# Kernel tuning notes

Hardware: AMD Instinct MI355X
Metric: run time of the kernel (lower is better)

## Reference

```python
import jax, jax.numpy as jnp
import numpy as np

N_NODES = 100000
N_EDGES = 1600000
IN_C, HID_C, OUT_C = 128, 128, 64


def setup_inputs() -> dict:
    key = jax.random.key(0)
    k = jax.random.split(key, 5)
    x = jax.random.normal(k[0], (N_NODES, IN_C), dtype=jnp.float32)
    edge_index = jax.random.randint(k[1], (2, N_EDGES), 0, N_NODES, dtype=jnp.int32)
    # Glorot-ish scaling for the GCNConv linear weights
    W1 = jax.random.normal(k[2], (IN_C, HID_C), dtype=jnp.float32) * (1.0 / np.sqrt(IN_C))
    b1 = jnp.zeros((HID_C,), dtype=jnp.float32)
    W2 = jax.random.normal(k[3], (HID_C, OUT_C), dtype=jnp.float32) * (1.0 / np.sqrt(HID_C))
    b2 = jnp.zeros((OUT_C,), dtype=jnp.float32)
    return {"x": x, "edge_index": edge_index, "W1": W1, "b1": b1, "W2": W2, "b2": b2}


def _gcn_conv(h, W, b, src, dst, deg_inv_sqrt, n):
    # h: [N, F_in] -> linear transform, then deg-normalized scatter-add over edges
    h = h @ W  # [N, F_out]
    norm = deg_inv_sqrt[src] * deg_inv_sqrt[dst]  # [E+N] (self-loops included)
    msgs = h[src] * norm[:, None]  # gather + scale
    out = jax.ops.segment_sum(msgs, dst, num_segments=n)  # scatter-add to dst
    return out + b


def reference(x, edge_index, W1, b1, W2, b2):
    n = x.shape[0]
    loops = jnp.arange(n, dtype=edge_index.dtype)
    src = jnp.concatenate([edge_index[0], loops])  # add self-loops (PyG default)
    dst = jnp.concatenate([edge_index[1], loops])
    deg = jax.ops.segment_sum(jnp.ones_like(dst, dtype=x.dtype), dst, num_segments=n)
    deg_inv_sqrt = jax.lax.rsqrt(deg)  # deg >= 1 due to self-loops

    h = _gcn_conv(x, W1, b1, src, dst, deg_inv_sqrt, n)
    h = jax.nn.relu(h)
    # F.dropout(training=False) is identity at inference
    h = _gcn_conv(h, W2, b2, src, dst, deg_inv_sqrt, n)
    return jax.nn.log_softmax(h, axis=1)
```

## Files before the change

### kernel.cpp

```cpp
#include <hip/hip_runtime.h>
#include <hip/hip_bf16.h>


typedef unsigned short ushortT;
typedef unsigned char ucharT;
typedef __attribute__((ext_vector_type(8))) short short8v;
typedef __attribute__((ext_vector_type(4))) float float4v;
typedef __attribute__((ext_vector_type(2))) float float2v;
typedef __attribute__((ext_vector_type(8))) unsigned short ushort8v;

__device__ __forceinline__ float bf2f(ushortT u) {
  union { unsigned int i; float f; } x;
  x.i = ((unsigned int)u) << 16;
  return x.f;
}

__device__ __forceinline__ ushortT f2bf(float f) {
  __hip_bfloat16 h = __float2bfloat16(f);
  return *(ushortT*)&h;
}

__device__ __forceinline__ ucharT f2fp8(float f) {
  unsigned int w = __builtin_amdgcn_cvt_pk_fp8_f32(f, f, 0, false);
  return (ucharT)(w & 0xff);
}

__device__ __forceinline__ void fp8x8_to_f32(unsigned int lo, unsigned int hi,
                                             float* f) {
  float2v p0 = __builtin_amdgcn_cvt_pk_f32_fp8(lo, false);
  float2v p1 = __builtin_amdgcn_cvt_pk_f32_fp8(lo, true);
  float2v p2 = __builtin_amdgcn_cvt_pk_f32_fp8(hi, false);
  float2v p3 = __builtin_amdgcn_cvt_pk_f32_fp8(hi, true);
  f[0] = p0[0]; f[1] = p0[1]; f[2] = p1[0]; f[3] = p1[1];
  f[4] = p2[0]; f[5] = p2[1]; f[6] = p3[0]; f[7] = p3[1];
}

__device__ __forceinline__ void fp8x4_to_f32(unsigned int w, float* f) {
  float2v p0 = __builtin_amdgcn_cvt_pk_f32_fp8(w, false);
  float2v p1 = __builtin_amdgcn_cvt_pk_f32_fp8(w, true);
  f[0] = p0[0]; f[1] = p0[1]; f[2] = p1[0]; f[3] = p1[1];
}

__device__ __forceinline__ bool probe_isbf(const void* xv) {
  const ushortT* xr = (const ushortT*)xv;
  const int lane = threadIdx.x & 63;
  float v = bf2f(xr[lane]);
  bool sane = isfinite(v) && fabsf(v) < 1e4f;
  return __ballot(sane) == ~0ull;
}

__global__ __launch_bounds__(256) void wprep_k(const void* __restrict__ W1v,
                                               const void* __restrict__ W2v,
                                               const void* __restrict__ xv,
                                               ushortT* __restrict__ Wt1,
                                               ushortT* __restrict__ Wt2) {
  const bool isbf = probe_isbf(xv);
  const int i = blockIdx.x * 256 + threadIdx.x;
  if (i < 16384) {
    int nn = i & 127, k = i >> 7;
    ushortT v = isbf ? ((const ushortT*)W1v)[k * 128 + nn]
                     : f2bf(((const float*)W1v)[k * 128 + nn]);
    Wt1[nn * 128 + k] = v;
  } else if (i < 24576) {
    int j = i - 16384;
    int nn = j & 63, k = j >> 6;
    ushortT v = isbf ? ((const ushortT*)W2v)[k * 64 + nn]
                     : f2bf(((const float*)W2v)[k * 64 + nn]);
    Wt2[nn * 128 + k] = v;
  }
}


__global__ __launch_bounds__(256) void bhist_k(const int* __restrict__ dst, int E, int B,
                                               int* __restrict__ gbc) {
  __shared__ int h[512];
  const int tid = threadIdx.x;
  for (int i = tid; i < B; i += 256) h[i] = 0;
  __syncthreads();
  const int i0 = blockIdx.x * 8192;
  const int iend = min(i0 + 8192, E);
  for (int i = i0 + tid; i < iend; i += 256) atomicAdd(&h[dst[i] >> 8], 1);
  __syncthreads();
  for (int i = tid; i < B; i += 256)
    if (h[i]) atomicAdd(&gbc[i], h[i]);
}

__global__ __launch_bounds__(256) void bscan_k(const int* __restrict__ gbc, int B,
                                               int* __restrict__ bbase,
                                               int* __restrict__ gcur) {
  __shared__ int p[256];
  const int t = threadIdx.x;
  int a = (2 * t < B) ? gbc[2 * t] : 0;
  int b = (2 * t + 1 < B) ? gbc[2 * t + 1] : 0;
  const int sum = a + b;
  p[t] = sum;
  __syncthreads();
  int run = sum;
  for (int off = 1; off < 256; off <<= 1) {
    int v = (t >= off) ? p[t - off] : 0;
    __syncthreads();
    run += v;
    p[t] = run;
    __syncthreads();
  }
  const int excl = run - sum;
  if (2 * t < B) { bbase[2 * t] = excl; gcur[2 * t] = excl; }
  if (2 * t + 1 < B) { bbase[2 * t + 1] = excl + a; gcur[2 * t + 1] = excl + a; }
}

__global__ __launch_bounds__(256) void bin_k(const int* __restrict__ srcv,
                                             const int* __restrict__ dstv, int E, int B,
                                             int* __restrict__ gcur,
                                             int* __restrict__ tmp) {
  __shared__ int hist[512];
  __shared__ int base[512];
  const int tid = threadIdx.x;
  const int i0 = blockIdx.x * 8192;
  const int iend = min(i0 + 8192, E);
  for (int i = tid; i < B; i += 256) hist[i] = 0;
  __syncthreads();
  for (int i = i0 + tid; i < iend; i += 256) atomicAdd(&hist[dstv[i] >> 8], 1);
  __syncthreads();
  for (int i = tid; i < B; i += 256) {
    int h = hist[i];
    base[i] = h ? atomicAdd(&gcur[i], h) : 0;
    hist[i] = 0;
  }
  __syncthreads();
  for (int i = i0 + tid; i < iend; i += 256) {
    int d = dstv[i];
    int s = srcv[i];
    int b = d >> 8;
    int l = atomicAdd(&hist[b], 1);
    tmp[base[b] + l] = s | ((d & 255) << 17);
  }
}

__global__ __launch_bounds__(256) void csr_k(const int* __restrict__ tmp,
                                             const int* __restrict__ bbase,
                                             const int* __restrict__ gbc, int n,
                                             int2* __restrict__ rpc,
                                             float* __restrict__ dis,
                                             int* __restrict__ col) {
  __shared__ int lhist[256];
  __shared__ int lexcl[256];
  const int b = blockIdx.x;
  const int tid = threadIdx.x;
  const int e0 = bbase[b];
  const int e1 = e0 + gbc[b];
  lhist[tid] = 0;
  __syncthreads();
  for (int i = e0 + tid; i < e1; i += 256) atomicAdd(&lhist[tmp[i] >> 17], 1);
  __syncthreads();
  const int v = lhist[tid];
  int run = v;
  lexcl[tid] = run;
  __syncthreads();
  for (int off = 1; off < 256; off <<= 1) {
    int t = (tid >= off) ? lexcl[tid - off] : 0;
    __syncthreads();
    run += t;
    lexcl[tid] = run;
    __syncthreads();
  }
  const int excl = run - v;
  const int node = (b << 8) + tid;
  if (node < n) {
    rpc[node] = make_int2(e0 + excl, v);
    dis[node] = rsqrtf((float)(v + 1));
  }
  lhist[tid] = 0;
  lexcl[tid] = excl;
  __syncthreads();
  for (int i = e0 + tid; i < e1; i += 256) {
    int p = tmp[i];
    int dloc = p >> 17;
    int s = p & 131071;
    int l = atomicAdd(&lhist[dloc], 1);
    col[e0 + lexcl[dloc] + l] = s;
  }
}

__global__ __launch_bounds__(512) void gemm1_k(const void* __restrict__ xv,
                                               const ushortT* __restrict__ Wt1,
                                               const float* __restrict__ dis,
                                               ucharT* __restrict__ Hb8, int n) {
  __shared__ ushortT sW[128 * 132];
  const bool isbf = probe_isbf(xv);
  const int tid = threadIdx.x;
  for (int i = tid; i < 4096; i += 512) {
    int nn = i >> 5, k4 = (i & 31) * 4;
    *(ushort4*)&sW[nn * 132 + k4] = *(const ushort4*)&Wt1[nn * 128 + k4];
  }
  __syncthreads();

  const int wave = tid >> 6;
  const int lane = tid & 63;
  const int m = lane & 15;
  const int quad = lane >> 4;
  const int row = blockIdx.x * 128 + wave * 16 + m;
  const int rowc = min(row, n - 1);

  float4v acc[8];
#pragma unroll
  for (int t = 0; t < 8; ++t) acc[t] = (float4v)(0.f);

  if (isbf) {
    const ushortT* xp = (const ushortT*)xv + (size_t)rowc * 128 + quad * 8;
#pragma unroll
    for (int kc = 0; kc < 4; ++kc) {
      short8v af = *(const short8v*)(xp + kc * 32);
#pragma unroll
      for (int nb = 0; nb < 8; ++nb) {
        short8v bf = *(const short8v*)&sW[(nb * 16 + m) * 132 + kc * 32 + quad * 8];
        acc[nb] = __builtin_amdgcn_mfma_f32_16x16x32_bf16(af, bf, acc[nb], 0, 0, 0);
      }
    }
  } else {
    const float* xp = (const float*)xv + (size_t)rowc * 128 + quad * 8;
#pragma unroll
    for (int kc = 0; kc < 4; ++kc) {
      float4 lo = *(const float4*)(xp + kc * 32);
      float4 hi = *(const float4*)(xp + kc * 32 + 4);
      short8v af;
      af[0] = (short)f2bf(lo.x); af[1] = (short)f2bf(lo.y);
      af[2] = (short)f2bf(lo.z); af[3] = (short)f2bf(lo.w);
      af[4] = (short)f2bf(hi.x); af[5] = (short)f2bf(hi.y);
      af[6] = (short)f2bf(hi.z); af[7] = (short)f2bf(hi.w);
#pragma unroll
      for (int nb = 0; nb < 8; ++nb) {
        short8v bf = *(const short8v*)&sW[(nb * 16 + m) * 132 + kc * 32 + quad * 8];
        acc[nb] = __builtin_amdgcn_mfma_f32_16x16x32_bf16(af, bf, acc[nb], 0, 0, 0);
      }
    }
  }

#pragma unroll
  for (int r = 0; r < 4; ++r) {
    int grow = blockIdx.x * 128 + wave * 16 + quad * 4 + r;
    if (grow <= n) {
      float sc = (grow < n) ? dis[grow] : 0.f;
#pragma unroll
      for (int nb = 0; nb < 8; ++nb)
        Hb8[(size_t)grow * 128 + nb * 16 + m] =
            (grow < n) ? f2fp8(sc * acc[nb][r]) : (ucharT)0;
    }
  }
}

__global__ __launch_bounds__(512) void mid_k(const ucharT* __restrict__ Hb8,
                                             const int* __restrict__ col,
                                             const int2* __restrict__ rpc,
                                             const float* __restrict__ dis,
                                             const void* __restrict__ b1v,
                                             const ushortT* __restrict__ Wt2,
                                             const void* __restrict__ xv,
                                             ucharT* __restrict__ H2b8, int n) {
  __shared__ ushortT sA[128 * 132];
  __shared__ ushortT sW[64 * 132];
  const bool isbf = probe_isbf(xv);
  const int tid = threadIdx.x;
  for (int i = tid; i < 2048; i += 512) {
    int nn = i >> 5, k4 = (i & 31) * 4;
    *(ushort4*)&sW[nn * 132 + k4] = *(const ushort4*)&Wt2[nn * 128 + k4];
  }

  const int lane = tid & 63;
  const int wave = tid >> 6;
  const int quad = lane >> 4;
  const int m = lane & 15;
  const int c8 = m * 8;
  const int node0 = blockIdx.x * 128;

  float b[8];
  if (isbf) {
    ushort8v bb = *(const ushort8v*)((const ushortT*)b1v + c8);
#pragma unroll
    for (int k = 0; k < 8; ++k) b[k] = bf2f(bb[k]);
  } else {
    const float* bf = (const float*)b1v + c8;
#pragma unroll
    for (int k = 0; k < 8; ++k) b[k] = bf[k];
  }

#pragma unroll
  for (int s = 0; s < 4; ++s) {
    const int lrow = s * 32 + wave * 4 + quad;
    const int node = node0 + lrow;
    const bool valid = node < n;
    const int nd = valid ? node : (n - 1);
    const int2 rc = rpc[nd];
    const int start = rc.x;
    const int cnt = valid ? rc.y : 0;
    const float din = dis[nd];
    const uint2 hsp =
        *(const uint2*)&Hb8[((unsigned)(valid ? node : n) << 7) + (unsigned)c8];

    int cmax = cnt;
    cmax = max(cmax, __shfl_xor(cmax, 16));
    cmax = max(cmax, __shfl_xor(cmax, 32));
    const int cmaxs = __builtin_amdgcn_readfirstlane(cmax);

    float2v acc[4];
#pragma unroll
    for (int k = 0; k < 4; ++k) acc[k] = (float2v)(0.f);

    for (int e = 0; e < cmaxs; e += 4) {
#pragma unroll
      for (int u = 0; u < 4; ++u) {
        const int ee = e + u;
        int sidx = col[start + ee];
        sidx = (ee < cnt) ? sidx : n;
        const uint2 h = *(const uint2*)&Hb8[((unsigned)sidx << 7) + (unsigned)c8];
        acc[0] += __builtin_amdgcn_cvt_pk_f32_fp8(h.x, false);
        acc[1] += __builtin_amdgcn_cvt_pk_f32_fp8(h.x, true);
        acc[2] += __builtin_amdgcn_cvt_pk_f32_fp8(h.y, false);
        acc[3] += __builtin_amdgcn_cvt_pk_f32_fp8(h.y, true);
      }
    }

    ushort8v o;
    if (valid) {
      float hs[8];
      fp8x8_to_f32(hsp.x, hsp.y, hs);
#pragma unroll
      for (int k = 0; k < 4; ++k) {
        o[2 * k]     = f2bf(fmaxf(fmaf(din, acc[k][0] + hs[2 * k],     b[2 * k]),     0.f));
        o[2 * k + 1] = f2bf(fmaxf(fmaf(din, acc[k][1] + hs[2 * k + 1], b[2 * k + 1]), 0.f));
      }
    } else {
#pragma unroll
      for (int k = 0; k < 8; ++k) o[k] = 0;
    }
    *(ushort8v*)&sA[lrow * 132 + c8] = o;
  }
  __syncthreads();

  float4v acc[4];
#pragma unroll
  for (int t = 0; t < 4; ++t) acc[t] = (float4v)(0.f);

  const int arow = wave * 16 + m;
#pragma unroll
  for (int kc = 0; kc < 4; ++kc) {
    short8v af = *(const short8v*)&sA[arow * 132 + kc * 32 + quad * 8];
#pragma unroll
    for (int nb = 0; nb < 4; ++nb) {
      short8v bf = *(const short8v*)&sW[(nb * 16 + m) * 132 + kc * 32 + quad * 8];
      acc[nb] = __builtin_amdgcn_mfma_f32_16x16x32_bf16(af, bf, acc[nb], 0, 0, 0);
    }
  }

#pragma unroll
  for (int r = 0; r < 4; ++r) {
    int grow = blockIdx.x * 128 + wave * 16 + quad * 4 + r;
    if (grow <= n) {
      float sc = (grow < n) ? dis[grow] : 0.f;
#pragma unroll
      for (int nb = 0; nb < 4; ++nb)
        H2b8[(size_t)grow * 64 + nb * 16 + m] =
            (grow < n) ? f2fp8(sc * acc[nb][r]) : (ucharT)0;
    }
  }
}

__global__ __launch_bounds__(256) void agg2_k(const ucharT* __restrict__ H2b8,
                                              const int* __restrict__ col,
                                              const int2* __restrict__ rpc,
                                              const float* __restrict__ dis,
                                              const void* __restrict__ b2v,
                                              const void* __restrict__ xv,
                                              void* __restrict__ outv, int n) {
  const bool isbf = probe_isbf(xv);
  const int tid = threadIdx.x;
  const int lane = tid & 63;
  const int wave = tid >> 6;
  const int quad = lane >> 4;
  const int m = lane & 15;
  const int c4 = m * 4;
  const int node = blockIdx.x * 16 + wave * 4 + quad;
  const bool valid = node < n;
  const int nd = valid ? node : (n - 1);

  const int2 rc = rpc[nd];
  const int start = rc.x;
  const int cnt = valid ? rc.y : 0;
  const float din = dis[nd];

  const unsigned int hsp =
      *(const unsigned int*)&H2b8[((unsigned)(valid ? node : n) << 6) + (unsigned)c4];
  float b[4];
  if (isbf) {
    ushort4 bb = *(const ushort4*)((const ushortT*)b2v + c4);
    b[0] = bf2f(bb.x); b[1] = bf2f(bb.y); b[2] = bf2f(bb.z); b[3] = bf2f(bb.w);
  } else {
    const float* bf = (const float*)b2v + c4;
#pragma unroll
    for (int k = 0; k < 4; ++k) b[k] = bf[k];
  }

  int cmax = cnt;
  cmax = max(cmax, __shfl_xor(cmax, 16));
  cmax = max(cmax, __shfl_xor(cmax, 32));
  const int cmaxs = __builtin_amdgcn_readfirstlane(cmax);

  float2v acc[2];
  acc[0] = (float2v)(0.f);
  acc[1] = (float2v)(0.f);

  for (int e = 0; e < cmaxs; e += 4) {
#pragma unroll
    for (int u = 0; u < 4; ++u) {
      const int ee = e + u;
      int s = col[start + ee];
      s = (ee < cnt) ? s : n;
      const unsigned int h = *(const unsigned int*)&H2b8[((unsigned)s << 6) + (unsigned)c4];
      acc[0] += __builtin_amdgcn_cvt_pk_f32_fp8(h, false);
      acc[1] += __builtin_amdgcn_cvt_pk_f32_fp8(h, true);
    }
  }

  float hs[4];
  fp8x4_to_f32(hsp, hs);
  float v[4];
  v[0] = fmaf(din, acc[0][0] + hs[0], b[0]);
  v[1] = fmaf(din, acc[0][1] + hs[1], b[1]);
  v[2] = fmaf(din, acc[1][0] + hs[2], b[2]);
  v[3] = fmaf(din, acc[1][1] + hs[3], b[3]);

  float mx = fmaxf(fmaxf(v[0], v[1]), fmaxf(v[2], v[3]));
  for (int off = 1; off < 16; off <<= 1) mx = fmaxf(mx, __shfl_xor(mx, off));
  float ssum = __expf(v[0] - mx) + __expf(v[1] - mx) + __expf(v[2] - mx) + __expf(v[3] - mx);
  for (int off = 1; off < 16; off <<= 1) ssum += __shfl_xor(ssum, off);
  const float lse = mx + __logf(ssum);

  if (valid) {
    if (isbf) {
      ushort4 o;
      o.x = f2bf(v[0] - lse); o.y = f2bf(v[1] - lse);
      o.z = f2bf(v[2] - lse); o.w = f2bf(v[3] - lse);
      *(ushort4*)((__hip_bfloat16*)outv + (size_t)node * 64 + c4) = o;
    } else {
      float4 o = make_float4(v[0] - lse, v[1] - lse, v[2] - lse, v[3] - lse);
      *(float4*)((float*)outv + (size_t)node * 64 + c4) = o;
    }
  }
}


extern "C" void kernel_launch(void* const* d_in, const int* in_sizes, int n_in,
                              void* d_out, int out_size, void* d_ws, size_t ws_size,
                              hipStream_t stream) {
  const void* x  = d_in[0];
  const int*  ei = (const int*)d_in[1];
  const void* W1 = d_in[2];
  const void* b1 = d_in[3];
  const void* W2 = d_in[4];
  const void* b2 = d_in[5];

  const int n = in_sizes[0] / 128;
  const int E = in_sizes[1] / 2;
  const int B = (n + 255) >> 8;
  const int* srcv = ei;
  const int* dstv = ei + E;

  char* p = (char*)d_ws;
  auto alloc = [&](size_t bytes) {
    char* q = p;
    p += (bytes + 255) & ~(size_t)255;
    return q;
  };
  ucharT* Hb8 = (ucharT*)alloc((size_t)(n + 1) * 128);
  ucharT* H2b8 = (ucharT*)alloc((size_t)(n + 1) * 64);
  float* dis = (float*)alloc((size_t)n * 4);
  int2* rpc = (int2*)alloc((size_t)n * 8);
  int* gbc = (int*)alloc(512 * 4);
  int* bbase = (int*)alloc(512 * 4);
  int* gcur = (int*)alloc(512 * 4);
  ushortT* Wt1 = (ushortT*)alloc(16384 * 2);
  ushortT* Wt2 = (ushortT*)alloc(8192 * 2);
  int* tmp = (int*)alloc((size_t)E * 4);
  int* col = (int*)alloc(((size_t)E + 4096) * 4);

  (void)hipMemsetAsync(gbc, 0, 512 * sizeof(int), stream);

  const int gChunks = (E + 8191) / 8192;

  wprep_k<<<96, 256, 0, stream>>>(W1, W2, x, Wt1, Wt2);
  bhist_k<<<gChunks, 256, 0, stream>>>(dstv, E, B, gbc);
  bscan_k<<<1, 256, 0, stream>>>(gbc, B, bbase, gcur);
  bin_k<<<gChunks, 256, 0, stream>>>(srcv, dstv, E, B, gcur, tmp);
  csr_k<<<B, 256, 0, stream>>>(tmp, bbase, gbc, n, rpc, dis, col);

  gemm1_k<<<(n + 128) / 128, 512, 0, stream>>>(x, Wt1, dis, Hb8, n);
  mid_k<<<(n + 128) / 128, 512, 0, stream>>>(Hb8, col, rpc, dis, b1, Wt2, x, H2b8, n);
  agg2_k<<<(n + 15) / 16, 256, 0, stream>>>(H2b8, col, rpc, dis, b2, x, d_out, n);
}
```

Before: 242.5 us.

## Interleave four nodes per lane group in aggregation and drop W2 LDS staging

Both aggregation kernels now give each 16-lane group four consecutive nodes and interleave their neighbor gathers in one loop, which puts more independent loads in flight. The loop bound is now the per-group maximum degree instead of a wave-wide one. mid_k no longer stages W2 in shared memory and reads the MFMA B operand straight from global memory, which cuts LDS use. Both kernels get occupancy hints via launch bounds, and agg2 launches a quarter as many blocks. Risks are higher register pressure, more global reads of W2, and divergent loop trip counts within a wave.

Result: slower. 332.0 us (+36.9%).

```diff
diff --git a/kernel.cpp b/kernel.cpp
--- a/kernel.cpp
+++ b/kernel.cpp
@@ -248,29 +248,25 @@
   }
 }
 
-__global__ __launch_bounds__(512) void mid_k(const ucharT* __restrict__ Hb8,
-                                             const int* __restrict__ col,
-                                             const int2* __restrict__ rpc,
-                                             const float* __restrict__ dis,
-                                             const void* __restrict__ b1v,
-                                             const ushortT* __restrict__ Wt2,
-                                             const void* __restrict__ xv,
-                                             ucharT* __restrict__ H2b8, int n) {
+__global__ __launch_bounds__(512, 6) void mid_k(const ucharT* __restrict__ Hb8,
+                                                const int* __restrict__ col,
+                                                const int2* __restrict__ rpc,
+                                                const float* __restrict__ dis,
+                                                const void* __restrict__ b1v,
+                                                const ushortT* __restrict__ Wt2,
+                                                const void* __restrict__ xv,
+                                                ucharT* __restrict__ H2b8, int n) {
   __shared__ ushortT sA[128 * 132];
-  __shared__ ushortT sW[64 * 132];
   const bool isbf = probe_isbf(xv);
   const int tid = threadIdx.x;
-  for (int i = tid; i < 2048; i += 512) {
-    int nn = i >> 5, k4 = (i & 31) * 4;
-    *(ushort4*)&sW[nn * 132 + k4] = *(const ushort4*)&Wt2[nn * 128 + k4];
-  }
-
   const int lane = tid & 63;
   const int wave = tid >> 6;
   const int quad = lane >> 4;
   const int m = lane & 15;
   const int c8 = m * 8;
   const int node0 = blockIdx.x * 128;
+  const int qid = wave * 4 + quad;
+  const int nb0 = node0 + qid * 4;
 
   float b[8];
   if (isbf) {
@@ -283,50 +279,52 @@
     for (int k = 0; k < 8; ++k) b[k] = bf[k];
   }
 
+  int startA[4], cntA[4];
+  float dinA[4];
+  uint2 hspA[4];
 #pragma unroll
   for (int s = 0; s < 4; ++s) {
-    const int lrow = s * 32 + wave * 4 + quad;
-    const int node = node0 + lrow;
+    const int node = nb0 + s;
     const bool valid = node < n;
     const int nd = valid ? node : (n - 1);
     const int2 rc = rpc[nd];
-    const int start = rc.x;
-    const int cnt = valid ? rc.y : 0;
-    const float din = dis[nd];
-    const uint2 hsp =
-        *(const uint2*)&Hb8[((unsigned)(valid ? node : n) << 7) + (unsigned)c8];
-
-    int cmax = cnt;
-    cmax = max(cmax, __shfl_xor(cmax, 16));
-    cmax = max(cmax, __shfl_xor(cmax, 32));
-    const int cmaxs = __builtin_amdgcn_readfirstlane(cmax);
-
-    float2v acc[4];
-#pragma unroll
-    for (int k = 0; k < 4; ++k) acc[k] = (float2v)(0.f);
-
-    for (int e = 0; e < cmaxs; e += 4) {
-#pragma unroll
-      for (int u = 0; u < 4; ++u) {
-        const int ee = e + u;
-        int sidx = col[start + ee];
-        sidx = (ee < cnt) ? sidx : n;
-        const uint2 h = *(const uint2*)&Hb8[((unsigned)sidx << 7) + (unsigned)c8];
-        acc[0] += __builtin_amdgcn_cvt_pk_f32_fp8(h.x, false);
-        acc[1] += __builtin_amdgcn_cvt_pk_f32_fp8(h.x, true);
-        acc[2] += __builtin_amdgcn_cvt_pk_f32_fp8(h.y, false);
-        acc[3] += __builtin_amdgcn_cvt_pk_f32_fp8(h.y, true);
-      }
-    }
-
+    startA[s] = rc.x;
+    cntA[s] = valid ? rc.y : 0;
+    dinA[s] = dis[nd];
+    hspA[s] = *(const uint2*)&Hb8[((unsigned)(valid ? node : n) << 7) + (unsigned)c8];
+  }
+  const int cmax = max(max(cntA[0], cntA[1]), max(cntA[2], cntA[3]));
+
+  float2v acc[4][4];
+#pragma unroll
+  for (int s = 0; s < 4; ++s)
+#pragma unroll
+    for (int k = 0; k < 4; ++k) acc[s][k] = (float2v)(0.f);
+
+  for (int e = 0; e < cmax; ++e) {
+#pragma unroll
+    for (int s = 0; s < 4; ++s) {
+      int sidx = col[startA[s] + e];
+      sidx = (e < cntA[s]) ? sidx : n;
+      const uint2 h = *(const uint2*)&Hb8[((unsigned)sidx << 7) + (unsigned)c8];
+      acc[s][0] += __builtin_amdgcn_cvt_pk_f32_fp8(h.x, false);
+      acc[s][1] += __builtin_amdgcn_cvt_pk_f32_fp8(h.x, true);
+      acc[s][2] += __builtin_amdgcn_cvt_pk_f32_fp8(h.y, false);
+      acc[s][3] += __builtin_amdgcn_cvt_pk_f32_fp8(h.y, true);
+    }
+  }
+
+#pragma unroll
+  for (int s = 0; s < 4; ++s) {
+    const int lrow = qid * 4 + s;
     ushort8v o;
-    if (valid) {
+    if (node0 + lrow < n) {
       float hs[8];
-      fp8x8_to_f32(hsp.x, hsp.y, hs);
+      fp8x8_to_f32(hspA[s].x, hspA[s].y, hs);
 #pragma unroll
       for (int k = 0; k < 4; ++k) {
-        o[2 * k]     = f2bf(fmaxf(fmaf(din, acc[k][0] + hs[2 * k],     b[2 * k]),     0.f));
-        o[2 * k + 1] = f2bf(fmaxf(fmaf(din, acc[k][1] + hs[2 * k + 1], b[2 * k + 1]), 0.f));
+        o[2 * k]     = f2bf(fmaxf(fmaf(dinA[s], acc[s][k][0] + hs[2 * k],     b[2 * k]),     0.f));
+        o[2 * k + 1] = f2bf(fmaxf(fmaf(dinA[s], acc[s][k][1] + hs[2 * k + 1], b[2 * k + 1]), 0.f));
       }
     } else {
 #pragma unroll
@@ -336,9 +334,9 @@
   }
   __syncthreads();
 
-  float4v acc[4];
-#pragma unroll
-  for (int t = 0; t < 4; ++t) acc[t] = (float4v)(0.f);
+  float4v acc2[4];
+#pragma unroll
+  for (int t = 0; t < 4; ++t) acc2[t] = (float4v)(0.f);
 
   const int arow = wave * 16 + m;
 #pragma unroll
@@ -346,8 +344,8 @@
     short8v af = *(const short8v*)&sA[arow * 132 + kc * 32 + quad * 8];
 #pragma unroll
     for (int nb = 0; nb < 4; ++nb) {
-      short8v bf = *(const short8v*)&sW[(nb * 16 + m) * 132 + kc * 32 + quad * 8];
-      acc[nb] = __builtin_amdgcn_mfma_f32_16x16x32_bf16(af, bf, acc[nb], 0, 0, 0);
+      short8v bf = *(const short8v*)&Wt2[(nb * 16 + m) * 128 + kc * 32 + quad * 8];
+      acc2[nb] = __builtin_amdgcn_mfma_f32_16x16x32_bf16(af, bf, acc2[nb], 0, 0, 0);
     }
   }
 
@@ -359,18 +357,18 @@
 #pragma unroll
       for (int nb = 0; nb < 4; ++nb)
         H2b8[(size_t)grow * 64 + nb * 16 + m] =
-            (grow < n) ? f2fp8(sc * acc[nb][r]) : (ucharT)0;
-    }
-  }
-}
-
-__global__ __launch_bounds__(256) void agg2_k(const ucharT* __restrict__ H2b8,
-                                              const int* __restrict__ col,
-                                              const int2* __restrict__ rpc,
-                                              const float* __restrict__ dis,
-                                              const void* __restrict__ b2v,
-                                              const void* __restrict__ xv,
-                                              void* __restrict__ outv, int n) {
+            (grow < n) ? f2fp8(sc * acc2[nb][r]) : (ucharT)0;
+    }
+  }
+}
+
+__global__ __launch_bounds__(256, 6) void agg2_k(const ucharT* __restrict__ H2b8,
+                                                 const int* __restrict__ col,
+                                                 const int2* __restrict__ rpc,
+                                                 const float* __restrict__ dis,
+                                                 const void* __restrict__ b2v,
+                                                 const void* __restrict__ xv,
+                                                 void* __restrict__ outv, int n) {
   const bool isbf = probe_isbf(xv);
   const int tid = threadIdx.x;
   const int lane = tid & 63;
@@ -378,17 +376,9 @@
   const int quad = lane >> 4;
   const int m = lane & 15;
   const int c4 = m * 4;
-  const int node = blockIdx.x * 16 + wave * 4 + quad;
-  const bool valid = node < n;
-  const int nd = valid ? node : (n - 1);
-
-  const int2 rc = rpc[nd];
-  const int start = rc.x;
-  const int cnt = valid ? rc.y : 0;
-  const float din = dis[nd];
-
-  const unsigned int hsp =
-      *(const unsigned int*)&H2b8[((unsigned)(valid ? node : n) << 6) + (unsigned)c4];
+  const int qid = wave * 4 + quad;
+  const int nb0 = blockIdx.x * 64 + qid * 4;
+
   float b[4];
   if (isbf) {
     ushort4 bb = *(const ushort4*)((const ushortT*)b2v + c4);
@@ -399,42 +389,63 @@
     for (int k = 0; k < 4; ++k) b[k] = bf[k];
   }
 
-  int cmax = cnt;
-  cmax = max(cmax, __shfl_xor(cmax, 16));
-  cmax = max(cmax, __shfl_xor(cmax, 32));
-  const int cmaxs = __builtin_amdgcn_readfirstlane(cmax);
-
-  float2v acc[2];
-  acc[0] = (float2v)(0.f);
-  acc[1] = (float2v)(0.f);
-
-  for (int e = 0; e < cmaxs; e += 4) {
-#pragma unroll
-    for (int u = 0; u < 4; ++u) {
-      const int ee = e + u;
-      int s = col[start + ee];
-      s = (ee < cnt) ? s : n;
-      const unsigned int h = *(const unsigned int*)&H2b8[((unsigned)s << 6) + (unsigned)c4];
-      acc[0] += __builtin_amdgcn_cvt_pk_f32_fp8(h, false);
-      acc[1] += __builtin_amdgcn_cvt_pk_f32_fp8(h, true);
-    }
-  }
-
-  float hs[4];
-  fp8x4_to_f32(hsp, hs);
-  float v[4];
-  v[0] = fmaf(din, acc[0][0] + hs[0], b[0]);
-  v[1] = fmaf(din, acc[0][1] + hs[1], b[1]);
-  v[2] = fmaf(din, acc[1][0] + hs[2], b[2]);
-  v[3] = fmaf(din, acc[1][1] + hs[3], b[3]);
-
-  float mx = fmaxf(fmaxf(v[0], v[1]), fmaxf(v[2], v[3]));
-  for (int off = 1; off < 16; off <<= 1) mx = fmaxf(mx, __shfl_xor(mx, off));
-  float ssum = __expf(v[0] - mx) + __expf(v[1] - mx) + __expf(v[2] - mx) + __expf(v[3] - mx);
-  for (int off = 1; off < 16; off <<= 1) ssum += __shfl_xor(ssum, off);
-  const float lse = mx + __logf(ssum);
-
-  if (valid) {
+  int startA[4], cntA[4];
+  float dinA[4];
+  unsigned int hspA[4];
+#pragma unroll
+  for (int s = 0; s < 4; ++s) {
+    const int node = nb0 + s;
+    const bool valid = node < n;
+    const int nd = valid ? node : (n - 1);
+    const int2 rc = rpc[nd];
+    startA[s] = rc.x;
+    cntA[s] = valid ? rc.y : 0;
+    dinA[s] = dis[nd];
+    hspA[s] = *(const unsigned int*)&H2b8[((unsigned)(valid ? node : n) << 6) + (unsigned)c4];
+  }
+  const int cmax = max(max(cntA[0], cntA[1]), max(cntA[2], cntA[3]));
+
+  float2v acc[4][2];
+#pragma unroll
+  for (int s = 0; s < 4; ++s) {
+    acc[s][0] = (float2v)(0.f);
+    acc[s][1] = (float2v)(0.f);
+  }
+
+  for (int e = 0; e < cmax; e += 2) {
+#pragma unroll
+    for (int s = 0; s < 4; ++s) {
+      int i0 = col[startA[s] + e];
+      int i1 = col[startA[s] + e + 1];
+      i0 = (e < cntA[s]) ? i0 : n;
+      i1 = (e + 1 < cntA[s]) ? i1 : n;
+      const unsigned int h0 = *(const unsigned int*)&H2b8[((unsigned)i0 << 6) + (unsigned)c4];
+      const unsigned int h1 = *(const unsigned int*)&H2b8[((unsigned)i1 << 6) + (unsigned)c4];
+      acc[s][0] += __builtin_amdgcn_cvt_pk_f32_fp8(h0, false);
+      acc[s][1] += __builtin_amdgcn_cvt_pk_f32_fp8(h0, true);
+      acc[s][0] += __builtin_amdgcn_cvt_pk_f32_fp8(h1, false);
+      acc[s][1] += __builtin_amdgcn_cvt_pk_f32_fp8(h1, true);
+    }
+  }
+
+#pragma unroll
+  for (int s = 0; s < 4; ++s) {
+    const int node = nb0 + s;
+    if (node >= n) continue;
+    float hs[4];
+    fp8x4_to_f32(hspA[s], hs);
+    float v[4];
+    v[0] = fmaf(dinA[s], acc[s][0][0] + hs[0], b[0]);
+    v[1] = fmaf(dinA[s], acc[s][0][1] + hs[1], b[1]);
+    v[2] = fmaf(dinA[s], acc[s][1][0] + hs[2], b[2]);
+    v[3] = fmaf(dinA[s], acc[s][1][1] + hs[3], b[3]);
+
+    float mx = fmaxf(fmaxf(v[0], v[1]), fmaxf(v[2], v[3]));
+    for (int off = 1; off < 16; off <<= 1) mx = fmaxf(mx, __shfl_xor(mx, off));
+    float ssum = __expf(v[0] - mx) + __expf(v[1] - mx) + __expf(v[2] - mx) + __expf(v[3] - mx);
+    for (int off = 1; off < 16; off <<= 1) ssum += __shfl_xor(ssum, off);
+    const float lse = mx + __logf(ssum);
+
     if (isbf) {
       ushort4 o;
       o.x = f2bf(v[0] - lse); o.y = f2bf(v[1] - lse);
@@ -494,5 +505,5 @@
 
   gemm1_k<<<(n + 128) / 128, 512, 0, stream>>>(x, Wt1, dis, Hb8, n);
   mid_k<<<(n + 128) / 128, 512, 0, stream>>>(Hb8, col, rpc, dis, b1, Wt2, x, H2b8, n);
-  agg2_k<<<(n + 15) / 16, 256, 0, stream>>>(H2b8, col, rpc, dis, b2, x, d_out, n);
-}
+  agg2_k<<<(n + 63) / 64, 256, 0, stream>>>(H2b8, col, rpc, dis, b2, x, d_out, n);
+}
```
